# Kernel optimization log

Measured on AMD Instinct MI355X. Metric: run time of the kernel, lower is better.

Reference implementation:

```python
import jax, jax.numpy as jnp
import numpy as np

C = 256          # conv_channels
C1 = C // 2      # 128
C2 = C // 4      # 64
G = 1            # relation_glimpse


def setup_inputs() -> dict:
    key = jax.random.key(0)
    ks = jax.random.split(key, 20)
    bs, Nr, in_dim, q_dim = 4, 256, 2052, 1024
    d_in = in_dim + 4  # pos (first 4 coords) re-appended
    s = 0.02
    inp = {
        "Q": jax.random.normal(ks[0], (bs, q_dim), jnp.float32),
        "X": jax.random.normal(ks[1], (bs, Nr, in_dim), jnp.float32),
        "Wv": jax.random.normal(ks[2], (d_in, C), jnp.float32) * s,
        "bv": jnp.zeros((C,), jnp.float32),
        "Wq": jax.random.normal(ks[3], (q_dim, C), jnp.float32) * s,
        "bq": jnp.zeros((C,), jnp.float32),
        # branch 0 (r_conv01/02/03): 1x1 convs == per-position dense
        "W01": jax.random.normal(ks[4], (C, C1), jnp.float32) * s,
        "b01": jnp.zeros((C1,), jnp.float32),
        "W02": jax.random.normal(ks[5], (C1, C2), jnp.float32) * s,
        "b02": jnp.zeros((C2,), jnp.float32),
        "W03": jax.random.normal(ks[6], (C2, G), jnp.float32) * s,
        "b03": jnp.zeros((G,), jnp.float32),
        # branch 1 (r_conv1/2/3): dilation on 1x1 kernels is a no-op
        "W1": jax.random.normal(ks[7], (C, C1), jnp.float32) * s,
        "b1": jnp.zeros((C1,), jnp.float32),
        "W2": jax.random.normal(ks[8], (C1, C2), jnp.float32) * s,
        "b2": jnp.zeros((C2,), jnp.float32),
        "W3": jax.random.normal(ks[9], (C2, G), jnp.float32) * s,
        "b3": jnp.zeros((G,), jnp.float32),
    }
    return inp


def _mlp3(P, Wa, ba, Wb, bb, Wc, bc):
    # P: [bs, Nr, Nr, C]; three 1x1-conv layers, ReLU after each (incl. last).
    h = jax.nn.relu(jnp.einsum("bijc,ck->bijk", P, Wa) + ba)
    h = jax.nn.relu(jnp.einsum("bijc,ck->bijk", h, Wb) + bb)
    h = jax.nn.relu(jnp.einsum("bijc,ck->bijk", h, Wc) + bc)
    return h[..., 0]  # [bs, Nr, Nr] (relation_glimpse == 1)


def _attn_map(h):
    # symmetrize, then softmax over all Nr*Nr positions
    s = h + jnp.swapaxes(h, 1, 2)
    bs, Nr, _ = s.shape
    return jax.nn.softmax(s.reshape(bs, Nr * Nr), axis=-1).reshape(bs, Nr, Nr)


def reference(Q, X, Wv, bv, Wq, bq, W01, b01, W02, b02, W03, b03,
              W1, b1, W2, b2, W3, b3):
    X_ = X
    # append pos (first 4 coords) -> [bs, Nr, in_dim+4]
    Xcat = jnp.concatenate([X, X[:, :, :4]], axis=2)
    Xp = jnp.einsum("bnd,dc->bnc", Xcat, Wv) + bv
    Qp = Q @ Wq + bq
    Xp = Xp + Qp[:, None, :]                       # [bs, Nr, C]
    P = Xp[:, None, :, :] * Xp[:, :, None, :]      # [bs, Nr, Nr, C] pairwise product
    m0 = _attn_map(_mlp3(P, W01, b01, W02, b02, W03, b03))
    m1 = _attn_map(_mlp3(P, W1, b1, W2, b2, W3, b3))
    # weighted aggregation with original features; /(2*glimpse), then sum over Nr
    rel = jnp.einsum("bij,bjd->bid", m0 + m1, X_) / (2.0 * G)
    return rel.sum(axis=1)  # [bs, in_dim]
```

## Files before the change

kernel.cpp:

```cpp
#include <hip/hip_runtime.h>
#include <hip/hip_bf16.h>

typedef __attribute__((ext_vector_type(8)))  short short8;
typedef __attribute__((ext_vector_type(4)))  float f32x4;
typedef __attribute__((ext_vector_type(16))) float f32x16;

#define NR 256
#define CC 256

__device__ __forceinline__ unsigned short f2bf(float x) {
    union { float f; unsigned int u; } v; v.f = x;
    unsigned int r = v.u + 0x7FFFu + ((v.u >> 16) & 1u);
    return (unsigned short)(r >> 16);
}

__device__ __forceinline__ unsigned int pk2bf(float a, float b) {
    __hip_bfloat162 h = __float22bfloat162_rn(make_float2(a, b));
    union { __hip_bfloat162 h; unsigned int u; } cv; cv.h = h;
    return cv.u;
}

__global__ __launch_bounds__(256) void setup_kernel(
    const float* __restrict__ Q, const float* __restrict__ Wq, float* __restrict__ Qpp,
    const float* __restrict__ Wv, unsigned short* __restrict__ wvp,
    const float* __restrict__ W01, const float* __restrict__ W1,
    const float* __restrict__ W02, const float* __restrict__ W2,
    unsigned short* __restrict__ wpa, unsigned short* __restrict__ wpb)
{
    __shared__ float tile[32][260];
    __shared__ float qs[256];
    const int bx = blockIdx.x;
    const int tid = threadIdx.x;

    if (bx < 16) {
        int ksl = bx & 3, b = bx >> 2;
        qs[tid] = Q[b * 1024 + ksl * 256 + tid];
        __syncthreads();
        float acc = 0.f;
        #pragma unroll 4
        for (int d = 0; d < 256; ++d) acc += qs[d] * Wq[(size_t)(ksl * 256 + d) * 256 + tid];
        Qpp[(ksl * 4 + b) * 256 + tid] = acc;
    } else if (bx < 81) {
        int ks = bx - 16;
        for (int idx = tid; idx < 32 * 256; idx += 256) {
            int cr = idx >> 8, n = idx & 255;
            int c = ks * 32 + cr;
            tile[cr][n] = (c < 2056) ? Wv[(size_t)c * 256 + n] : 0.f;
        }
        __syncthreads();
        #pragma unroll
        for (int q = 0; q < 4; ++q) {
            int t2 = tid * 4 + q;
            int nt = t2 >> 6, l = t2 & 63;
            int gg = l >> 4, jj = l & 15;
            short8 s;
            #pragma unroll
            for (int e = 0; e < 8; ++e)
                s[e] = (short)f2bf(tile[gg * 8 + e][nt * 16 + jj]);
            *(short8*)&wvp[((size_t)(ks * 16 + nt) * 64 + l) * 8] = s;
        }
    } else {
        int t = (bx - 81) * 256 + tid;
        if (t < 65536) {
            int e = t & 7, l = (t >> 3) & 63, ks = (t >> 9) & 15, nt = (t >> 13) & 3, br = (t >> 15) & 1;
            int cc = ks * 16 + (l >> 5) * 8 + e;
            int n = nt * 32 + (l & 31);
            const float* W = br ? W1 : W01;
            wpa[t] = f2bf(W[cc * 128 + n]);
        } else {
            int t2 = t - 65536;
            int e = t2 & 7, l = (t2 >> 3) & 63, ks = (t2 >> 9) & 7, nt = (t2 >> 12) & 1, br = (t2 >> 13) & 1;
            int cc = ks * 16 + (l >> 5) * 8 + e;
            int n = nt * 32 + (l & 31);
            const float* W = br ? W2 : W02;
            wpb[t2] = f2bf(W[cc * 64 + n]);
        }
    }
}

__global__ __launch_bounds__(512) void xp_kernel(
    const float* __restrict__ X, const unsigned short* __restrict__ wvp,
    const float* __restrict__ bv, const float* __restrict__ bq,
    const float* __restrict__ Qpp, float* __restrict__ Xp)
{
    __shared__ f32x4 red[8][4][65];
    const int tid = threadIdx.x;
    const int w = tid >> 6;
    const int lane = tid & 63;
    const int g = lane >> 4, j16v = lane & 15;
    const int mt = blockIdx.x;
    const int bn = blockIdx.y;
    const int b  = blockIdx.z;

    const int i0 = mt * 16;
    const float* xrow = X + ((size_t)(b * NR) + (i0 + j16v)) * 2052;

    f32x4 acc[4] = {};

    for (int ks = w; ks < 64; ks += 8) {
        const int c0 = ks * 32 + g * 8;
        float4 xa = *(const float4*)(xrow + c0);
        float4 xb = *(const float4*)(xrow + c0 + 4);
        union { short8 s; unsigned int u[4]; } af;
        af.u[0] = pk2bf(xa.x, xa.y);
        af.u[1] = pk2bf(xa.z, xa.w);
        af.u[2] = pk2bf(xb.x, xb.y);
        af.u[3] = pk2bf(xb.z, xb.w);
        #pragma unroll
        for (int nt = 0; nt < 4; ++nt) {
            short8 bf = ((const short8*)wvp)[(size_t)(ks * 16 + bn * 4 + nt) * 64 + lane];
            acc[nt] = __builtin_amdgcn_mfma_f32_16x16x32_bf16(af.s, bf, acc[nt], 0, 0, 0);
        }
    }
    if (w == 0) {
        float xv[8];
        #pragma unroll
        for (int e = 0; e < 8; ++e) {
            int q = g * 8 + e;
            int csrc = (q < 4) ? (2048 + q) : (q - 4);
            xv[e] = xrow[csrc];
        }
        union { short8 s; unsigned int u[4]; } af;
        af.u[0] = pk2bf(xv[0], xv[1]);
        af.u[1] = pk2bf(xv[2], xv[3]);
        af.u[2] = pk2bf(xv[4], xv[5]);
        af.u[3] = pk2bf(xv[6], xv[7]);
        #pragma unroll
        for (int nt = 0; nt < 4; ++nt) {
            short8 bf = ((const short8*)wvp)[(size_t)(64 * 16 + bn * 4 + nt) * 64 + lane];
            acc[nt] = __builtin_amdgcn_mfma_f32_16x16x32_bf16(af.s, bf, acc[nt], 0, 0, 0);
        }
    }
    #pragma unroll
    for (int nt = 0; nt < 4; ++nt) red[w][nt][lane] = acc[nt];
    __syncthreads();

    #pragma unroll
    for (int idx = tid; idx < 1024; idx += 512) {
        int nt = idx >> 8, rem = idx & 255;
        int l = rem & 63, reg = rem >> 6;
        float rsum = 0.f;
        #pragma unroll
        for (int ww = 0; ww < 8; ++ww) rsum += red[ww][nt][l][reg];
        int gg = l >> 4, jj = l & 15;
        int n = bn * 64 + nt * 16 + jj;
        float base = bv[n] + bq[n] + Qpp[b * 256 + n] + Qpp[(4 + b) * 256 + n]
                   + Qpp[(8 + b) * 256 + n] + Qpp[(12 + b) * 256 + n];
        int row = i0 + gg * 4 + reg;
        Xp[((b * NR) + row) * CC + n] = rsum + base;
    }
}

__global__ __launch_bounds__(512, 2) void pairs_kernel(
    const float* __restrict__ Xp,
    const unsigned short* __restrict__ wpa,
    const unsigned short* __restrict__ wpb,
    const float* __restrict__ b01, const float* __restrict__ b02,
    const float* __restrict__ b03,
    const float* __restrict__ b1,  const float* __restrict__ b2,
    const float* __restrict__ b3,
    const float* __restrict__ W03, const float* __restrict__ W3,
    float* __restrict__ colpart, float* __restrict__ rowpart)
{
    __shared__ __align__(16) unsigned short lds_wa[32768];
    __shared__ __align__(16) float lds_si[2048];
    __shared__ __align__(16) float lds_bias1[128];
    __shared__ __align__(16) float lds_bias2[64];
    __shared__ __align__(16) float lds_w3[64];
    __shared__ float lds_c[8][33];

    const int tid = threadIdx.x;
    const int wave = tid >> 6;
    const int lane = tid & 63;
    const int hi = lane >> 5;
    const int j32 = lane & 31;

    int bx = blockIdx.x;
    int b = bx / 288;
    int r = bx - b * 288;
    int br = r / 144;
    int u = r - br * 144;
    int k = 0, off = 0;
    while (k < 7) {
        int cnt = 4 * (8 - k);
        if (u < off + cnt) break;
        off += cnt; ++k;
    }
    int rel = u - off;
    int it8 = 4 * k + rel / (8 - k);
    int jt  = k + rel % (8 - k);

    const int i = it8 * 8 + wave;
    const int blk = br * 4 + b;
    const int j0 = jt * 32;
    const int j = j0 + j32;

    *(float4*)&lds_si[wave * 256 + lane * 4] =
        *(const float4*)&Xp[((b * NR) + i) * CC + lane * 4];

    {
        const uint4* g1 = (const uint4*)(wpa + (size_t)br * 32768);
        uint4* s1 = (uint4*)lds_wa;
        #pragma unroll
        for (int kk = 0; kk < 8; ++kk) s1[kk * 512 + tid] = g1[kk * 512 + tid];
        if (tid < 128) lds_bias1[tid] = br ? b1[tid] : b01[tid];
        else if (tid < 192) lds_bias2[tid - 128] = br ? b2[tid - 128] : b02[tid - 128];
        else if (tid < 256) lds_w3[tid - 192] = br ? W3[tid - 192] : W03[tid - 192];
    }
    __syncthreads();
    const float b3v = br ? b3[0] : b03[0];
    const float* si = lds_si + wave * 256;
    const float* xr = Xp + ((size_t)(b * NR) + j) * CC;

    f32x16 acc1[4];
    #pragma unroll
    for (int t = 0; t < 4; ++t) {
        #pragma unroll
        for (int q = 0; q < 4; ++q) {
            const float* bb = &lds_bias1[t * 32 + q * 8 + hi * 4];
            acc1[t][q * 4 + 0] = bb[0];
            acc1[t][q * 4 + 1] = bb[1];
            acc1[t][q * 4 + 2] = bb[2];
            acc1[t][q * 4 + 3] = bb[3];
        }
    }

    short8 bfr[8];
    #pragma unroll
    for (int ksl = 0; ksl < 8; ++ksl) {
        const int c0 = ksl * 16 + hi * 8;
        float4 xa = *(const float4*)(xr + c0);
        float4 xb = *(const float4*)(xr + c0 + 4);
        float4 sa = *(const float4*)(si + c0);
        float4 sb = *(const float4*)(si + c0 + 4);
        union { short8 s; unsigned int uu[4]; } f;
        f.uu[0] = pk2bf(xa.x * sa.x, xa.y * sa.y);
        f.uu[1] = pk2bf(xa.z * sa.z, xa.w * sa.w);
        f.uu[2] = pk2bf(xb.x * sb.x, xb.y * sb.y);
        f.uu[3] = pk2bf(xb.z * sb.z, xb.w * sb.w);
        bfr[ksl] = f.s;
    }
    #pragma unroll
    for (int ksl = 0; ksl < 8; ++ksl) {
        const short8 bb = bfr[ksl];
        #pragma unroll
        for (int t = 0; t < 4; ++t) {
            short8 wf = ((const short8*)lds_wa)[(t * 16 + ksl) * 64 + lane];
            acc1[t] = __builtin_amdgcn_mfma_f32_32x32x16_bf16(wf, bb, acc1[t], 0, 0, 0);
        }
    }

    #pragma unroll
    for (int ksl = 0; ksl < 8; ++ksl) {
        const int c0 = (8 + ksl) * 16 + hi * 8;
        float4 xa = *(const float4*)(xr + c0);
        float4 xb = *(const float4*)(xr + c0 + 4);
        float4 sa = *(const float4*)(si + c0);
        float4 sb = *(const float4*)(si + c0 + 4);
        union { short8 s; unsigned int uu[4]; } f;
        f.uu[0] = pk2bf(xa.x * sa.x, xa.y * sa.y);
        f.uu[1] = pk2bf(xa.z * sa.z, xa.w * sa.w);
        f.uu[2] = pk2bf(xb.x * sb.x, xb.y * sb.y);
        f.uu[3] = pk2bf(xb.z * sb.z, xb.w * sb.w);
        bfr[ksl] = f.s;
    }
    #pragma unroll
    for (int ksl = 0; ksl < 8; ++ksl) {
        const short8 bb = bfr[ksl];
        #pragma unroll
        for (int t = 0; t < 4; ++t) {
            short8 wf = ((const short8*)lds_wa)[(t * 16 + 8 + ksl) * 64 + lane];
            acc1[t] = __builtin_amdgcn_mfma_f32_32x32x16_bf16(wf, bb, acc1[t], 0, 0, 0);
        }
    }

    f32x16 acc2[2];
    #pragma unroll
    for (int nt = 0; nt < 2; ++nt) {
        #pragma unroll
        for (int q = 0; q < 4; ++q) {
            const float* bb = &lds_bias2[nt * 32 + q * 8 + hi * 4];
            acc2[nt][q * 4 + 0] = bb[0];
            acc2[nt][q * 4 + 1] = bb[1];
            acc2[nt][q * 4 + 2] = bb[2];
            acc2[nt][q * 4 + 3] = bb[3];
        }
    }
    const short8* wb = (const short8*)wpb + (size_t)br * 1024;

    short8 w2r[8];
    #pragma unroll
    for (int q = 0; q < 4; ++q) {
        w2r[q]     = wb[q * 64 + lane];
        w2r[4 + q] = wb[(8 + q) * 64 + lane];
    }
    #pragma unroll
    for (int t = 0; t < 2; ++t) {
        #pragma unroll
        for (int s = 0; s < 2; ++s) {
            const int bse = s * 8;
            float rA0 = fmaxf(acc1[t][bse + 0], 0.f), rA1 = fmaxf(acc1[t][bse + 1], 0.f);
            float rA2 = fmaxf(acc1[t][bse + 2], 0.f), rA3 = fmaxf(acc1[t][bse + 3], 0.f);
            float rB0 = fmaxf(acc1[t][bse + 4], 0.f), rB1 = fmaxf(acc1[t][bse + 5], 0.f);
            float rB2 = fmaxf(acc1[t][bse + 6], 0.f), rB3 = fmaxf(acc1[t][bse + 7], 0.f);
            unsigned int uA0 = pk2bf(rA0, rA1), uA1 = pk2bf(rA2, rA3);
            unsigned int uB0 = pk2bf(rB0, rB1), uB1 = pk2bf(rB2, rB3);
            unsigned int pA0 = __shfl_xor(uA0, 32, 64), pA1 = __shfl_xor(uA1, 32, 64);
            unsigned int pB0 = __shfl_xor(uB0, 32, 64), pB1 = __shfl_xor(uB1, 32, 64);
            union { short8 s8; unsigned int uu[4]; } B2;
            B2.uu[0] = hi ? pB0 : uA0;
            B2.uu[1] = hi ? pB1 : uA1;
            B2.uu[2] = hi ? uB0 : pA0;
            B2.uu[3] = hi ? uB1 : pA1;
            const int ks2 = 2 * t + s;
            acc2[0] = __builtin_amdgcn_mfma_f32_32x32x16_bf16(w2r[ks2], B2.s8, acc2[0], 0, 0, 0);
            acc2[1] = __builtin_amdgcn_mfma_f32_32x32x16_bf16(w2r[4 + ks2], B2.s8, acc2[1], 0, 0, 0);
        }
    }
    #pragma unroll
    for (int q = 0; q < 4; ++q) {
        w2r[q]     = wb[(4 + q) * 64 + lane];
        w2r[4 + q] = wb[(12 + q) * 64 + lane];
    }
    #pragma unroll
    for (int t = 2; t < 4; ++t) {
        #pragma unroll
        for (int s = 0; s < 2; ++s) {
            const int bse = s * 8;
            float rA0 = fmaxf(acc1[t][bse + 0], 0.f), rA1 = fmaxf(acc1[t][bse + 1], 0.f);
            float rA2 = fmaxf(acc1[t][bse + 2], 0.f), rA3 = fmaxf(acc1[t][bse + 3], 0.f);
            float rB0 = fmaxf(acc1[t][bse + 4], 0.f), rB1 = fmaxf(acc1[t][bse + 5], 0.f);
            float rB2 = fmaxf(acc1[t][bse + 6], 0.f), rB3 = fmaxf(acc1[t][bse + 7], 0.f);
            unsigned int uA0 = pk2bf(rA0, rA1), uA1 = pk2bf(rA2, rA3);
            unsigned int uB0 = pk2bf(rB0, rB1), uB1 = pk2bf(rB2, rB3);
            unsigned int pA0 = __shfl_xor(uA0, 32, 64), pA1 = __shfl_xor(uA1, 32, 64);
            unsigned int pB0 = __shfl_xor(uB0, 32, 64), pB1 = __shfl_xor(uB1, 32, 64);
            union { short8 s8; unsigned int uu[4]; } B2;
            B2.uu[0] = hi ? pB0 : uA0;
            B2.uu[1] = hi ? pB1 : uA1;
            B2.uu[2] = hi ? uB0 : pA0;
            B2.uu[3] = hi ? uB1 : pA1;
            const int ks2 = 2 * t + s - 4;
            acc2[0] = __builtin_amdgcn_mfma_f32_32x32x16_bf16(w2r[ks2], B2.s8, acc2[0], 0, 0, 0);
            acc2[1] = __builtin_amdgcn_mfma_f32_32x32x16_bf16(w2r[4 + ks2], B2.s8, acc2[1], 0, 0, 0);
        }
    }

    float part = 0.f;
    #pragma unroll
    for (int nt = 0; nt < 2; ++nt) {
        #pragma unroll
        for (int q = 0; q < 4; ++q) {
            const float* wv = &lds_w3[nt * 32 + q * 8 + hi * 4];
            part += fmaxf(acc2[nt][q * 4 + 0], 0.f) * wv[0];
            part += fmaxf(acc2[nt][q * 4 + 1], 0.f) * wv[1];
            part += fmaxf(acc2[nt][q * 4 + 2], 0.f) * wv[2];
            part += fmaxf(acc2[nt][q * 4 + 3], 0.f) * wv[3];
        }
    }
    part += __shfl_xor(part, 32, 64);
    const float h3 = fmaxf(part + b3v, 0.f);
    const float E = __expf(2.f * h3);
    const float Ec = (j >= i) ? E : 0.f;
    float Er = (j >  i) ? E : 0.f;

    Er += __shfl_xor(Er, 1, 64);
    Er += __shfl_xor(Er, 2, 64);
    Er += __shfl_xor(Er, 4, 64);
    Er += __shfl_xor(Er, 8, 64);
    Er += __shfl_xor(Er, 16, 64);
    Er += __shfl_xor(Er, 32, 64);
    if (lane == 0)
        rowpart[((size_t)blk * NR + i) * 8 + jt] = 0.5f * Er;

    if (!hi) lds_c[wave][j32] = Ec;
    __syncthreads();
    if (tid < 32) {
        float c = 0.f;
        #pragma unroll
        for (int wv2 = 0; wv2 < 8; ++wv2) c += lds_c[wv2][tid];
        colpart[(size_t)blk * 4608 + 64 * jt * (jt + 1) + tid * (4 * jt + 4) + it8] = c;
    }
}

__global__ __launch_bounds__(256) void agg_part_kernel(
    const float* __restrict__ X, const float* __restrict__ colpart,
    const float* __restrict__ rowpart, float* __restrict__ apart)
{
    const int dc = blockIdx.x, b = blockIdx.y, jc = blockIdx.z;
    const int tid = threadIdx.x;
    __shared__ float csh[2][256];
    __shared__ float red2[2][256];
    __shared__ float wc[32];

    {
        const int jt = tid >> 5, j32l = tid & 31;
        const int cnt = 4 * jt + 4;
        #pragma unroll
        for (int brx = 0; brx < 2; ++brx) {
            const int blk = brx * 4 + b;
            float cs = 0.f;
            const float* cp = colpart + (size_t)blk * 4608 + 64 * jt * (jt + 1) + j32l * cnt;
            for (int it2 = 0; it2 < cnt; ++it2) cs += cp[it2];
            const float* rp = rowpart + ((size_t)blk * NR + tid) * 8;
            for (int q = jt; q < 8; ++q) cs += rp[q];
            csh[brx][tid] = cs;
            red2[brx][tid] = cs;
        }
    }
    __syncthreads();
    for (int s = 128; s > 0; s >>= 1) {
        if (tid < s) { red2[0][tid] += red2[0][tid + s]; red2[1][tid] += red2[1][tid + s]; }
        __syncthreads();
    }
    if (tid < 32) {
        int jx = jc * 32 + tid;
        wc[tid] = 0.5f * (csh[0][jx] / red2[0][0] + csh[1][jx] / red2[1][0]);
    }
    __syncthreads();

    const int d = dc * 256 + tid;
    if (d < 2052) {
        const float* xp = X + (size_t)b * NR * 2052 + (size_t)jc * 32 * 2052 + d;
        float a0 = 0.f, a1 = 0.f, a2 = 0.f, a3 = 0.f;
        for (int rr = 0; rr < 32; rr += 4) {
            a0 += wc[rr + 0] * xp[(size_t)(rr + 0) * 2052];
            a1 += wc[rr + 1] * xp[(size_t)(rr + 1) * 2052];
            a2 += wc[rr + 2] * xp[(size_t)(rr + 2) * 2052];
            a3 += wc[rr + 3] * xp[(size_t)(rr + 3) * 2052];
        }
        apart[(size_t)(jc * 4 + b) * 2304 + d] = (a0 + a1) + (a2 + a3);
    }
}

__global__ __launch_bounds__(256) void agg_final_kernel(
    const float* __restrict__ apart, float* __restrict__ out)
{
    const int dc = blockIdx.x, b = blockIdx.y;
    const int d = dc * 256 + threadIdx.x;
    if (d < 2052) {
        float s = 0.f;
        #pragma unroll
        for (int jc = 0; jc < 8; ++jc) s += apart[(size_t)(jc * 4 + b) * 2304 + d];
        out[b * 2052 + d] = s;
    }
}

extern "C" void kernel_launch(void* const* d_in, const int* in_sizes, int n_in,
                              void* d_out, int out_size, void* d_ws, size_t ws_size,
                              hipStream_t stream) {
    const float* Q   = (const float*)d_in[0];
    const float* X   = (const float*)d_in[1];
    const float* Wv  = (const float*)d_in[2];
    const float* bv  = (const float*)d_in[3];
    const float* Wq  = (const float*)d_in[4];
    const float* bq  = (const float*)d_in[5];
    const float* W01 = (const float*)d_in[6];
    const float* b01 = (const float*)d_in[7];
    const float* W02 = (const float*)d_in[8];
    const float* b02 = (const float*)d_in[9];
    const float* W03 = (const float*)d_in[10];
    const float* b03 = (const float*)d_in[11];
    const float* W1  = (const float*)d_in[12];
    const float* b1  = (const float*)d_in[13];
    const float* W2  = (const float*)d_in[14];
    const float* b2  = (const float*)d_in[15];
    const float* W3  = (const float*)d_in[16];
    const float* b3  = (const float*)d_in[17];

    char* ws = (char*)d_ws;
    float* Xp   = (float*)(ws + 0);
    float* Qpp  = (float*)(ws + 1048576);
    unsigned short* wpa = (unsigned short*)(ws + 1073152);
    unsigned short* wpb = (unsigned short*)(ws + 1204224);
    float* colpart = (float*)(ws + 1236992);
    float* rowpart = (float*)(ws + 1384448);
    unsigned short* wvp = (unsigned short*)(ws + 1236992);
    float* apart = (float*)(ws + 0);
    float* out = (float*)d_out;

    setup_kernel<<<401, 256, 0, stream>>>(Q, Wq, Qpp, Wv, wvp,
                                          W01, W1, W02, W2, wpa, wpb);
    xp_kernel<<<dim3(16, 4, 4), 512, 0, stream>>>(X, wvp, bv, bq, Qpp, Xp);
    pairs_kernel<<<1152, 512, 0, stream>>>(Xp, wpa, wpb, b01, b02, b03,
                                           b1, b2, b3, W03, W3, colpart, rowpart);
    agg_part_kernel<<<dim3(9, 4, 8), 256, 0, stream>>>(X, colpart, rowpart, apart);
    agg_final_kernel<<<dim3(9, 4), 256, 0, stream>>>(apart, out);
}
```

Baseline: 100.9 us.

## Process two column tiles per pairs block to amortize weight staging

Each pairs_kernel block now loops over up to two 32-column j-tiles, reusing the LDS-staged first-layer weights, biases and the i-row of Xp. This cuts the grid from 1152 to 640 blocks and reduces the repeated 64KB weight load into LDS. The loop body also loads all 16 B-fragments and all 16 second-layer weight fragments at once, which raises register pressure. It adds an extra barrier per iteration and leaves some blocks with only one tile, so load across blocks is uneven.

Result: slower. 122.7 us (+21.6%).

```diff
diff --git a/kernel.cpp b/kernel.cpp
--- a/kernel.cpp
+++ b/kernel.cpp
@@ -176,24 +176,23 @@
     const int j32 = lane & 31;
 
     int bx = blockIdx.x;
-    int b = bx / 288;
-    int r = bx - b * 288;
-    int br = r / 144;
-    int u = r - br * 144;
+    int b = bx / 160;
+    int r = bx - b * 160;
+    int br = r / 80;
+    int u = r - br * 80;
     int k = 0, off = 0;
     while (k < 7) {
-        int cnt = 4 * (8 - k);
+        int cnt = 4 * ((9 - k) / 2);
         if (u < off + cnt) break;
         off += cnt; ++k;
     }
     int rel = u - off;
-    int it8 = 4 * k + rel / (8 - k);
-    int jt  = k + rel % (8 - k);
+    int bpi = (9 - k) / 2;
+    int it8 = 4 * k + rel / bpi;
+    int jt_a = k + 2 * (rel % bpi);
 
     const int i = it8 * 8 + wave;
     const int blk = br * 4 + b;
-    const int j0 = jt * 32;
-    const int j = j0 + j32;
 
     *(float4*)&lds_si[wave * 256 + lane * 4] =
         *(const float4*)&Xp[((b * NR) + i) * CC + lane * 4];
@@ -210,176 +209,132 @@
     __syncthreads();
     const float b3v = br ? b3[0] : b03[0];
     const float* si = lds_si + wave * 256;
-    const float* xr = Xp + ((size_t)(b * NR) + j) * CC;
-
-    f32x16 acc1[4];
-    #pragma unroll
-    for (int t = 0; t < 4; ++t) {
-        #pragma unroll
-        for (int q = 0; q < 4; ++q) {
-            const float* bb = &lds_bias1[t * 32 + q * 8 + hi * 4];
-            acc1[t][q * 4 + 0] = bb[0];
-            acc1[t][q * 4 + 1] = bb[1];
-            acc1[t][q * 4 + 2] = bb[2];
-            acc1[t][q * 4 + 3] = bb[3];
-        }
-    }
-
-    short8 bfr[8];
-    #pragma unroll
-    for (int ksl = 0; ksl < 8; ++ksl) {
-        const int c0 = ksl * 16 + hi * 8;
-        float4 xa = *(const float4*)(xr + c0);
-        float4 xb = *(const float4*)(xr + c0 + 4);
-        float4 sa = *(const float4*)(si + c0);
-        float4 sb = *(const float4*)(si + c0 + 4);
-        union { short8 s; unsigned int uu[4]; } f;
-        f.uu[0] = pk2bf(xa.x * sa.x, xa.y * sa.y);
-        f.uu[1] = pk2bf(xa.z * sa.z, xa.w * sa.w);
-        f.uu[2] = pk2bf(xb.x * sb.x, xb.y * sb.y);
-        f.uu[3] = pk2bf(xb.z * sb.z, xb.w * sb.w);
-        bfr[ksl] = f.s;
-    }
-    #pragma unroll
-    for (int ksl = 0; ksl < 8; ++ksl) {
-        const short8 bb = bfr[ksl];
+
+    #pragma unroll 1
+    for (int pj = 0; pj < 2; ++pj) {
+        const int jt = jt_a + pj;
+        if (jt >= 8) break;
+        const int j0 = jt * 32;
+        const int j = j0 + j32;
+        const float* xr = Xp + ((size_t)(b * NR) + j) * CC;
+
+        short8 bfr[16];
+        #pragma unroll
+        for (int ks = 0; ks < 16; ++ks) {
+            const int c0 = ks * 16 + hi * 8;
+            float4 xa = *(const float4*)(xr + c0);
+            float4 xb = *(const float4*)(xr + c0 + 4);
+            float4 sa = *(const float4*)(si + c0);
+            float4 sb = *(const float4*)(si + c0 + 4);
+            union { short8 s; unsigned int uu[4]; } f;
+            f.uu[0] = pk2bf(xa.x * sa.x, xa.y * sa.y);
+            f.uu[1] = pk2bf(xa.z * sa.z, xa.w * sa.w);
+            f.uu[2] = pk2bf(xb.x * sb.x, xb.y * sb.y);
+            f.uu[3] = pk2bf(xb.z * sb.z, xb.w * sb.w);
+            bfr[ks] = f.s;
+        }
+
+        f32x16 acc1[4];
         #pragma unroll
         for (int t = 0; t < 4; ++t) {
-            short8 wf = ((const short8*)lds_wa)[(t * 16 + ksl) * 64 + lane];
-            acc1[t] = __builtin_amdgcn_mfma_f32_32x32x16_bf16(wf, bb, acc1[t], 0, 0, 0);
-        }
-    }
-
-    #pragma unroll
-    for (int ksl = 0; ksl < 8; ++ksl) {
-        const int c0 = (8 + ksl) * 16 + hi * 8;
-        float4 xa = *(const float4*)(xr + c0);
-        float4 xb = *(const float4*)(xr + c0 + 4);
-        float4 sa = *(const float4*)(si + c0);
-        float4 sb = *(const float4*)(si + c0 + 4);
-        union { short8 s; unsigned int uu[4]; } f;
-        f.uu[0] = pk2bf(xa.x * sa.x, xa.y * sa.y);
-        f.uu[1] = pk2bf(xa.z * sa.z, xa.w * sa.w);
-        f.uu[2] = pk2bf(xb.x * sb.x, xb.y * sb.y);
-        f.uu[3] = pk2bf(xb.z * sb.z, xb.w * sb.w);
-        bfr[ksl] = f.s;
-    }
-    #pragma unroll
-    for (int ksl = 0; ksl < 8; ++ksl) {
-        const short8 bb = bfr[ksl];
+            #pragma unroll
+            for (int q = 0; q < 4; ++q) {
+                const float* bb = &lds_bias1[t * 32 + q * 8 + hi * 4];
+                acc1[t][q * 4 + 0] = bb[0];
+                acc1[t][q * 4 + 1] = bb[1];
+                acc1[t][q * 4 + 2] = bb[2];
+                acc1[t][q * 4 + 3] = bb[3];
+            }
+        }
+        #pragma unroll
+        for (int ks = 0; ks < 16; ++ks) {
+            const short8 bb = bfr[ks];
+            #pragma unroll
+            for (int t = 0; t < 4; ++t) {
+                short8 wf = ((const short8*)lds_wa)[(t * 16 + ks) * 64 + lane];
+                acc1[t] = __builtin_amdgcn_mfma_f32_32x32x16_bf16(wf, bb, acc1[t], 0, 0, 0);
+            }
+        }
+
+        short8 w2r[16];
+        {
+            const short8* wb = (const short8*)wpb + (size_t)br * 1024;
+            #pragma unroll
+            for (int q = 0; q < 16; ++q) w2r[q] = wb[q * 64 + lane];
+        }
+
+        f32x16 acc2[2];
+        #pragma unroll
+        for (int nt = 0; nt < 2; ++nt) {
+            #pragma unroll
+            for (int q = 0; q < 4; ++q) {
+                const float* bb = &lds_bias2[nt * 32 + q * 8 + hi * 4];
+                acc2[nt][q * 4 + 0] = bb[0];
+                acc2[nt][q * 4 + 1] = bb[1];
+                acc2[nt][q * 4 + 2] = bb[2];
+                acc2[nt][q * 4 + 3] = bb[3];
+            }
+        }
         #pragma unroll
         for (int t = 0; t < 4; ++t) {
-            short8 wf = ((const short8*)lds_wa)[(t * 16 + 8 + ksl) * 64 + lane];
-            acc1[t] = __builtin_amdgcn_mfma_f32_32x32x16_bf16(wf, bb, acc1[t], 0, 0, 0);
-        }
-    }
-
-    f32x16 acc2[2];
-    #pragma unroll
-    for (int nt = 0; nt < 2; ++nt) {
-        #pragma unroll
-        for (int q = 0; q < 4; ++q) {
-            const float* bb = &lds_bias2[nt * 32 + q * 8 + hi * 4];
-            acc2[nt][q * 4 + 0] = bb[0];
-            acc2[nt][q * 4 + 1] = bb[1];
-            acc2[nt][q * 4 + 2] = bb[2];
-            acc2[nt][q * 4 + 3] = bb[3];
-        }
-    }
-    const short8* wb = (const short8*)wpb + (size_t)br * 1024;
-
-    short8 w2r[8];
-    #pragma unroll
-    for (int q = 0; q < 4; ++q) {
-        w2r[q]     = wb[q * 64 + lane];
-        w2r[4 + q] = wb[(8 + q) * 64 + lane];
-    }
-    #pragma unroll
-    for (int t = 0; t < 2; ++t) {
-        #pragma unroll
-        for (int s = 0; s < 2; ++s) {
-            const int bse = s * 8;
-            float rA0 = fmaxf(acc1[t][bse + 0], 0.f), rA1 = fmaxf(acc1[t][bse + 1], 0.f);
-            float rA2 = fmaxf(acc1[t][bse + 2], 0.f), rA3 = fmaxf(acc1[t][bse + 3], 0.f);
-            float rB0 = fmaxf(acc1[t][bse + 4], 0.f), rB1 = fmaxf(acc1[t][bse + 5], 0.f);
-            float rB2 = fmaxf(acc1[t][bse + 6], 0.f), rB3 = fmaxf(acc1[t][bse + 7], 0.f);
-            unsigned int uA0 = pk2bf(rA0, rA1), uA1 = pk2bf(rA2, rA3);
-            unsigned int uB0 = pk2bf(rB0, rB1), uB1 = pk2bf(rB2, rB3);
-            unsigned int pA0 = __shfl_xor(uA0, 32, 64), pA1 = __shfl_xor(uA1, 32, 64);
-            unsigned int pB0 = __shfl_xor(uB0, 32, 64), pB1 = __shfl_xor(uB1, 32, 64);
-            union { short8 s8; unsigned int uu[4]; } B2;
-            B2.uu[0] = hi ? pB0 : uA0;
-            B2.uu[1] = hi ? pB1 : uA1;
-            B2.uu[2] = hi ? uB0 : pA0;
-            B2.uu[3] = hi ? uB1 : pA1;
-            const int ks2 = 2 * t + s;
-            acc2[0] = __builtin_amdgcn_mfma_f32_32x32x16_bf16(w2r[ks2], B2.s8, acc2[0], 0, 0, 0);
-            acc2[1] = __builtin_amdgcn_mfma_f32_32x32x16_bf16(w2r[4 + ks2], B2.s8, acc2[1], 0, 0, 0);
-        }
-    }
-    #pragma unroll
-    for (int q = 0; q < 4; ++q) {
-        w2r[q]     = wb[(4 + q) * 64 + lane];
-        w2r[4 + q] = wb[(12 + q) * 64 + lane];
-    }
-    #pragma unroll
-    for (int t = 2; t < 4; ++t) {
-        #pragma unroll
-        for (int s = 0; s < 2; ++s) {
-            const int bse = s * 8;
-            float rA0 = fmaxf(acc1[t][bse + 0], 0.f), rA1 = fmaxf(acc1[t][bse + 1], 0.f);
-            float rA2 = fmaxf(acc1[t][bse + 2], 0.f), rA3 = fmaxf(acc1[t][bse + 3], 0.f);
-            float rB0 = fmaxf(acc1[t][bse + 4], 0.f), rB1 = fmaxf(acc1[t][bse + 5], 0.f);
-            float rB2 = fmaxf(acc1[t][bse + 6], 0.f), rB3 = fmaxf(acc1[t][bse + 7], 0.f);
-            unsigned int uA0 = pk2bf(rA0, rA1), uA1 = pk2bf(rA2, rA3);
-            unsigned int uB0 = pk2bf(rB0, rB1), uB1 = pk2bf(rB2, rB3);
-            unsigned int pA0 = __shfl_xor(uA0, 32, 64), pA1 = __shfl_xor(uA1, 32, 64);
-            unsigned int pB0 = __shfl_xor(uB0, 32, 64), pB1 = __shfl_xor(uB1, 32, 64);
-            union { short8 s8; unsigned int uu[4]; } B2;
-            B2.uu[0] = hi ? pB0 : uA0;
-            B2.uu[1] = hi ? pB1 : uA1;
-            B2.uu[2] = hi ? uB0 : pA0;
-            B2.uu[3] = hi ? uB1 : pA1;
-            const int ks2 = 2 * t + s - 4;
-            acc2[0] = __builtin_amdgcn_mfma_f32_32x32x16_bf16(w2r[ks2], B2.s8, acc2[0], 0, 0, 0);
-            acc2[1] = __builtin_amdgcn_mfma_f32_32x32x16_bf16(w2r[4 + ks2], B2.s8, acc2[1], 0, 0, 0);
-        }
-    }
-
-    float part = 0.f;
-    #pragma unroll
-    for (int nt = 0; nt < 2; ++nt) {
-        #pragma unroll
-        for (int q = 0; q < 4; ++q) {
-            const float* wv = &lds_w3[nt * 32 + q * 8 + hi * 4];
-            part += fmaxf(acc2[nt][q * 4 + 0], 0.f) * wv[0];
-            part += fmaxf(acc2[nt][q * 4 + 1], 0.f) * wv[1];
-            part += fmaxf(acc2[nt][q * 4 + 2], 0.f) * wv[2];
-            part += fmaxf(acc2[nt][q * 4 + 3], 0.f) * wv[3];
-        }
-    }
-    part += __shfl_xor(part, 32, 64);
-    const float h3 = fmaxf(part + b3v, 0.f);
-    const float E = __expf(2.f * h3);
-    const float Ec = (j >= i) ? E : 0.f;
-    float Er = (j >  i) ? E : 0.f;
-
-    Er += __shfl_xor(Er, 1, 64);
-    Er += __shfl_xor(Er, 2, 64);
-    Er += __shfl_xor(Er, 4, 64);
-    Er += __shfl_xor(Er, 8, 64);
-    Er += __shfl_xor(Er, 16, 64);
-    Er += __shfl_xor(Er, 32, 64);
-    if (lane == 0)
-        rowpart[((size_t)blk * NR + i) * 8 + jt] = 0.5f * Er;
-
-    if (!hi) lds_c[wave][j32] = Ec;
-    __syncthreads();
-    if (tid < 32) {
-        float c = 0.f;
-        #pragma unroll
-        for (int wv2 = 0; wv2 < 8; ++wv2) c += lds_c[wv2][tid];
-        colpart[(size_t)blk * 4608 + 64 * jt * (jt + 1) + tid * (4 * jt + 4) + it8] = c;
+            #pragma unroll
+            for (int s = 0; s < 2; ++s) {
+                const int bse = s * 8;
+                float rA0 = fmaxf(acc1[t][bse + 0], 0.f), rA1 = fmaxf(acc1[t][bse + 1], 0.f);
+                float rA2 = fmaxf(acc1[t][bse + 2], 0.f), rA3 = fmaxf(acc1[t][bse + 3], 0.f);
+                float rB0 = fmaxf(acc1[t][bse + 4], 0.f), rB1 = fmaxf(acc1[t][bse + 5], 0.f);
+                float rB2 = fmaxf(acc1[t][bse + 6], 0.f), rB3 = fmaxf(acc1[t][bse + 7], 0.f);
+                unsigned int uA0 = pk2bf(rA0, rA1), uA1 = pk2bf(rA2, rA3);
+                unsigned int uB0 = pk2bf(rB0, rB1), uB1 = pk2bf(rB2, rB3);
+                unsigned int pA0 = __shfl_xor(uA0, 32, 64), pA1 = __shfl_xor(uA1, 32, 64);
+                unsigned int pB0 = __shfl_xor(uB0, 32, 64), pB1 = __shfl_xor(uB1, 32, 64);
+                union { short8 s8; unsigned int uu[4]; } B2;
+                B2.uu[0] = hi ? pB0 : uA0;
+                B2.uu[1] = hi ? pB1 : uA1;
+                B2.uu[2] = hi ? uB0 : pA0;
+                B2.uu[3] = hi ? uB1 : pA1;
+                const int ks2 = 2 * t + s;
+                acc2[0] = __builtin_amdgcn_mfma_f32_32x32x16_bf16(w2r[ks2], B2.s8, acc2[0], 0, 0, 0);
+                acc2[1] = __builtin_amdgcn_mfma_f32_32x32x16_bf16(w2r[8 + ks2], B2.s8, acc2[1], 0, 0, 0);
+            }
+        }
+
+        float part = 0.f;
+        #pragma unroll
+        for (int nt = 0; nt < 2; ++nt) {
+            #pragma unroll
+            for (int q = 0; q < 4; ++q) {
+                const float* wv = &lds_w3[nt * 32 + q * 8 + hi * 4];
+                part += fmaxf(acc2[nt][q * 4 + 0], 0.f) * wv[0];
+                part += fmaxf(acc2[nt][q * 4 + 1], 0.f) * wv[1];
+                part += fmaxf(acc2[nt][q * 4 + 2], 0.f) * wv[2];
+                part += fmaxf(acc2[nt][q * 4 + 3], 0.f) * wv[3];
+            }
+        }
+        part += __shfl_xor(part, 32, 64);
+        const float h3 = fmaxf(part + b3v, 0.f);
+        const float E = __expf(2.f * h3);
+        const float Ec = (j >= i) ? E : 0.f;
+        float Er = (j >  i) ? E : 0.f;
+
+        Er += __shfl_xor(Er, 1, 64);
+        Er += __shfl_xor(Er, 2, 64);
+        Er += __shfl_xor(Er, 4, 64);
+        Er += __shfl_xor(Er, 8, 64);
+        Er += __shfl_xor(Er, 16, 64);
+        Er += __shfl_xor(Er, 32, 64);
+        if (lane == 0)
+            rowpart[((size_t)blk * NR + i) * 8 + jt] = 0.5f * Er;
+
+        if (!hi) lds_c[wave][j32] = Ec;
+        __syncthreads();
+        if (tid < 32) {
+            float c = 0.f;
+            #pragma unroll
+            for (int wv2 = 0; wv2 < 8; ++wv2) c += lds_c[wv2][tid];
+            colpart[(size_t)blk * 4608 + 64 * jt * (jt + 1) + tid * (4 * jt + 4) + it8] = c;
+        }
+        __syncthreads();
     }
 }
 
@@ -482,8 +437,8 @@
     setup_kernel<<<401, 256, 0, stream>>>(Q, Wq, Qpp, Wv, wvp,
                                           W01, W1, W02, W2, wpa, wpb);
     xp_kernel<<<dim3(16, 4, 4), 512, 0, stream>>>(X, wvp, bv, bq, Qpp, Xp);
-    pairs_kernel<<<1152, 512, 0, stream>>>(Xp, wpa, wpb, b01, b02, b03,
-                                           b1, b2, b3, W03, W3, colpart, rowpart);
+    pairs_kernel<<<640, 512, 0, stream>>>(Xp, wpa, wpb, b01, b02, b03,
+                                          b1, b2, b3, W03, W3, colpart, rowpart);
     agg_part_kernel<<<dim3(9, 4, 8), 256, 0, stream>>>(X, colpart, rowpart, apart);
     agg_final_kernel<<<dim3(9, 4), 256, 0, stream>>>(apart, out);
 }
```
